# Performance work log

Measured on AMD Instinct MI355X. Metric: run time of the kernel, lower is better.

Reference implementation:

```python
import jax, jax.numpy as jnp
import numpy as np

B, N, M = 2, 256, 256  # batch items, bboxes per item, feature dim (output_channel)
BLOCKS = 2             # graph_conv_block_num


def _conv2d(x, w, b):
    # x: [C,H,W], w: [O,I,kh,kw] -> [O,H,W], SAME padding, stride 1
    y = jax.lax.conv_general_dilated(x[None], w, (1, 1), 'SAME',
                                     dimension_numbers=('NCHW', 'OIHW', 'NCHW'))
    return y[0] + b[:, None, None]


def setup_inputs() -> dict:
    key = jax.random.key(0)
    ks = jax.random.split(key, 8)
    s = 0.02  # small init to keep activations tame through conv stack
    return {
        'edge_feats': jax.random.normal(ks[0], (B, N, N, 7), jnp.float32),
        'node_feats': jax.random.normal(ks[1], (B, N, M), jnp.float32),
        'adapter_w': jax.random.normal(ks[2], (M, 7, 1, 1), jnp.float32) * s,
        'adapter_b': jnp.zeros((M,), jnp.float32),
        'conv0_w': jax.random.normal(ks[3], (M, 3 * M, 3, 3), jnp.float32) * s,
        'conv0_b': jnp.zeros((M,), jnp.float32),
        'conv1_w': jax.random.normal(ks[4], (M, M, 3, 3), jnp.float32) * s,
        'conv1_b': jnp.zeros((M,), jnp.float32),
        'last_w': jax.random.normal(ks[5], (M, M, 3, 3), jnp.float32) * s,
        'last_b': jnp.zeros((M,), jnp.float32),
        'att_w': jax.random.normal(ks[6], (1, M, 1, 1), jnp.float32) * s,
        'att_b': jnp.zeros((1,), jnp.float32),
    }


def reference(edge_feats, node_feats, adapter_w, adapter_b, conv0_w, conv0_b,
              conv1_w, conv1_b, last_w, last_b, att_w, att_b):
    def one(e, n):
        # e: [N,N,7], n: [N,M]
        edge = _conv2d(jnp.transpose(e, (2, 0, 1)), adapter_w, adapter_b)  # [M,N,N]
        node = n
        for _ in range(BLOCKS):  # conv weights shared across blocks, as in torch
            nT = node.T  # [M,N]
            # channel layout at (i,j): [node_i | edge_ij | node_j]
            feat = jnp.concatenate([
                jnp.broadcast_to(nT[:, :, None], (M, N, N)),
                edge,
                jnp.broadcast_to(nT[:, None, :], (M, N, N)),
            ], axis=0)  # [3M,N,N]
            feat = jax.nn.relu(_conv2d(feat, conv0_w, conv0_b))
            feat = jax.nn.relu(_conv2d(feat, conv1_w, conv1_b))
            # edge attention: 1x1 conv -> leaky_relu -> softmax over j -> weighted sum
            att = jax.nn.leaky_relu(_conv2d(feat, att_w, att_b))   # [1,N,N]
            coeff = jax.nn.softmax(att, axis=-1)                   # softmax over last dim
            node = jnp.sum(coeff * feat, axis=-1).T                # [N,M]
            edge = jax.nn.relu(_conv2d(feat, last_w, last_b))      # [M,N,N]
        return node, jnp.transpose(edge, (1, 2, 0))  # [N,M], [N,N,M]
    return jax.vmap(one)(edge_feats, node_feats)
```

## Files before the change

kernel.cpp:

```cpp
#include <hip/hip_runtime.h>
#include <hip/hip_bf16.h>

typedef __hip_bfloat16 bf16;
typedef __attribute__((ext_vector_type(8))) short s16x8;
typedef __attribute__((ext_vector_type(4))) float f32x4;

__device__ __forceinline__ float b2f(bf16 x) { return __bfloat162float(x); }
__device__ __forceinline__ bf16 f2b(float x) { return __float2bfloat16(x); }

#define BARRIER() do { asm volatile("" ::: "memory"); \
                       __builtin_amdgcn_s_barrier();  \
                       asm volatile("" ::: "memory"); } while (0)

__global__ __launch_bounds__(256) void fill_sentinel(float* out, int n) {
  int idx = blockIdx.x * 256 + threadIdx.x;
  if (idx < n) out[idx] = 100.0f;
}

__global__ __launch_bounds__(256) void zero_fill(bf16* z) {
  z[blockIdx.x * 256 + threadIdx.x] = f2b(0.f);
}

__global__ __launch_bounds__(256) void pack_w(const float* __restrict__ c0w,
                                              const float* __restrict__ c1w,
                                              const float* __restrict__ lw,
                                              bf16* wp0, bf16* wp1, bf16* wp2, bf16* wnp) {
  const int SEG = 9 * 256 * 256;
  int idx = blockIdx.x * 256 + threadIdx.x;
  if (idx < 3 * SEG) {
    int which = idx / SEG, r = idx % SEG;
    int s = r >> 16, o = (r >> 8) & 255, c = r & 255;
    int ky = s / 3, kx = s - 3 * ky;
    if (which == 0)      wp0[r] = f2b(c0w[(((size_t)o * 768 + 256 + c) * 3 + ky) * 3 + kx]);
    else if (which == 1) wp1[r] = f2b(c1w[(((size_t)o * 256 + c) * 3 + ky) * 3 + kx]);
    else                 wp2[r] = f2b(lw [(((size_t)o * 256 + c) * 3 + ky) * 3 + kx]);
  } else {
    int r = idx - 3 * SEG;
    int m = r & 255, c = (r >> 8) & 255, tt = r >> 16;
    int ot = tt % 3, t2 = (tt / 3) % 3, p = tt / 9;
    int ky, kx, cin;
    if (p == 0) { kx = t2; ky = ot; cin = c; }
    else        { ky = t2; kx = ot; cin = 512 + c; }
    wnp[r] = f2b(c0w[(((size_t)m * 768 + cin) * 3 + ky) * 3 + kx]);
  }
}

__global__ __launch_bounds__(256) void adapter_k(const float* __restrict__ e,
                                                 const float* __restrict__ aw,
                                                 const float* __restrict__ ab,
                                                 bf16* __restrict__ E) {
  int i = blockIdx.x;
  int m = threadIdx.x;
  __shared__ float se[256 * 7];
  const size_t rb = (size_t)i * (256 * 7);
  for (int idx = m; idx < 256 * 7; idx += 256) se[idx] = e[rb + idx];
  __syncthreads();
  float w[7];
#pragma unroll
  for (int c = 0; c < 7; ++c) w[c] = aw[m * 7 + c];
  float bias = ab[m];
  bf16* ob = E + (size_t)i * 65536 + m;
  for (int j = 0; j < 256; ++j) {
    const float* ej = se + j * 7;
    float a = bias;
#pragma unroll
    for (int c = 0; c < 7; ++c) a += w[c] * ej[c];
    ob[(size_t)j * 256] = f2b(a);
  }
}

template <typename T>
__global__ __launch_bounds__(256) void node_terms(const T* __restrict__ nd,
                                                  const bf16* __restrict__ wnp,
                                                  float* __restrict__ TT) {
  int bid = blockIdx.x;
  int chunk = bid & 63;
  int t = (bid >> 6) % 3;
  int p = bid / 192;
  int tid = threadIdx.x;
  __shared__ float snd[6][256];
  int pos0 = chunk * 4;
  for (int idx = tid; idx < 6 * 256; idx += 256) {
    int r = idx >> 8, c = idx & 255;
    int gp = pos0 - 1 + r;
    snd[r][c] = (gp >= 0 && gp < 256) ? (float)nd[(size_t)gp * 256 + c] : 0.f;
  }
  __syncthreads();
  float acc[4] = {0.f, 0.f, 0.f, 0.f};
  const bf16* wb = wnp + (size_t)((p * 3 + t) * 3) * 65536 + tid;
  for (int c = 0; c < 256; ++c) {
    float w0 = b2f(wb[(size_t)c * 256]);
    float w1 = b2f(wb[(size_t)(65536 + c * 256)]);
    float w2 = b2f(wb[(size_t)(2 * 65536 + c * 256)]);
#pragma unroll
    for (int ii = 0; ii < 4; ++ii)
      acc[ii] += w0 * snd[ii][c] + w1 * snd[ii + 1][c] + w2 * snd[ii + 2][c];
  }
  float* o = TT + (((size_t)(p * 3 + t) * 256 + pos0) * 256) + tid;
#pragma unroll
  for (int ii = 0; ii < 4; ++ii) o[(size_t)ii * 256] = acc[ii];
}

template <int EPI, int F32OUT>
__global__ __launch_bounds__(512, 1)
void conv3x3_k(const bf16* __restrict__ inb, const bf16* __restrict__ wpack,
               const float* __restrict__ bias, void* __restrict__ outv,
               const float* __restrict__ TT, const bf16* __restrict__ zrow) {
  __shared__ __align__(16) char lds[131072];
  const int bid = blockIdx.x;
  const int i = ((bid & 7) << 5) + (bid >> 3);
  const int tid = threadIdx.x;
  const int lane = tid & 63, wid = tid >> 6;
  const int wr = wid >> 2, wc = wid & 3;
  const int lo = lane & 15, hi = lane >> 4;
  const int xlane = tid >> 3;
  const int sw = ((tid & 7) ^ (xlane & 7)) << 3;
  const int g16 = (tid & 7) << 4;

  const int gxk0 = (hi ^ (lo & 7)) << 4;
  const int gxk1 = ((4 + hi) ^ (lo & 7)) << 4;
  const int aJ0 = (wr * 64 + lo) * 128 + gxk0;
  const int aJ1 = (wr * 64 + lo) * 128 + gxk1;
  const int bBase = ((wc & 1) * 64 + lo) * 128 + 65536 + (wc >> 1) * 16384;
  const int bJ0 = bBase + gxk0;
  const int bJ1 = bBase + gxk1;

  f32x4 acc00[4][2], acc01[4][2], acc10[4][2], acc11[4][2];
  const f32x4 z = {0.f, 0.f, 0.f, 0.f};
#pragma unroll
  for (int mf = 0; mf < 4; ++mf)
#pragma unroll
    for (int nf = 0; nf < 2; ++nf) { acc00[mf][nf] = z; acc01[mf][nf] = z;
                                     acc10[mf][nf] = z; acc11[mf][nf] = z; }
  s16x8 afA[4][2], bf0[2][2], bf1[2][2];
  s16x8 gi[4], gw[4];

  const bf16* rows0 = (i >= 1)   ? inb + (size_t)(i - 1) * 65536 : zrow;
  const bf16* rows1 = inb + (size_t)i * 65536;
  const bf16* rows2 = (i <= 254) ? inb + (size_t)(i + 1) * 65536 : zrow;

  auto ISSUE = [&](int t) {
    const int ky = (t >= 24) ? 2 : ((t >= 12) ? 1 : 0);
    const int rem = t - ky * 12;
    const int kx = rem >> 2, cc = rem & 3;
    const bf16* rowp = (ky == 0) ? rows0 : (ky == 1 ? rows1 : rows2);
    const int s = ky * 3 + kx;
#pragma unroll
    for (int r = 0; r < 4; ++r) {
      const int px = r * 64 + xlane;
      const int j = px + kx - 1;
      const bf16* src = (j >= 0 && j <= 255)
          ? rowp + ((size_t)j << 8) + cc * 64 + sw
          : zrow + sw;
      gi[r] = *(const s16x8*)src;
      gw[r] = *(const s16x8*)(wpack + ((size_t)s << 16) +
                              (((size_t)(r * 64 + xlane)) << 8) + cc * 64 + sw);
    }
  };
  auto WRITE_STAGE = [&](int par) {
#pragma unroll
    for (int r = 0; r < 4; ++r) {
      const int px = r * 64 + xlane;
      *(s16x8*)(lds + par * 32768 + px * 128 + g16) = gi[r];
      *(s16x8*)(lds + 65536 + par * 32768 + px * 128 + g16) = gw[r];
    }
  };
  auto LD_A = [&](int par, int mh) {
#pragma unroll
    for (int mf = 0; mf < 4; ++mf) {
      afA[mf][0] = *(const s16x8*)(lds + aJ0 + mf * 2048 + mh * 16384 + par * 32768);
      afA[mf][1] = *(const s16x8*)(lds + aJ1 + mf * 2048 + mh * 16384 + par * 32768);
    }
  };
  auto LD_B = [&](int par, int nh, s16x8 (&dst)[2][2]) {
#pragma unroll
    for (int nf = 0; nf < 2; ++nf) {
      dst[nf][0] = *(const s16x8*)(lds + bJ0 + nh * 4096 + nf * 2048 + par * 32768);
      dst[nf][1] = *(const s16x8*)(lds + bJ1 + nh * 4096 + nf * 2048 + par * 32768);
    }
  };

#define MMA_Q(ACC, BFR)                                                       \
  __builtin_amdgcn_s_setprio(1);                                              \
  _Pragma("unroll") for (int kk = 0; kk < 2; ++kk)                            \
  _Pragma("unroll") for (int mf = 0; mf < 4; ++mf)                            \
  _Pragma("unroll") for (int nf = 0; nf < 2; ++nf)                            \
    ACC[mf][nf] = __builtin_amdgcn_mfma_f32_16x16x32_bf16(                    \
        afA[mf][kk], BFR[nf][kk], ACC[mf][nf], 0, 0, 0);                      \
  __builtin_amdgcn_s_setprio(0);

  ISSUE(0);
  asm volatile("s_waitcnt vmcnt(0)" ::: "memory");
  WRITE_STAGE(0);
  asm volatile("s_waitcnt lgkmcnt(0)" ::: "memory");
  BARRIER();

#pragma unroll 1
  for (int t = 0; t < 36; ++t) {
    const int p = t & 1;
    if (t < 35) ISSUE(t + 1);
    LD_A(p, 0); LD_B(p, 0, bf0); LD_B(p, 1, bf1);
    MMA_Q(acc00, bf0);
    MMA_Q(acc01, bf1);
    LD_A(p, 1);
    MMA_Q(acc10, bf0);
    MMA_Q(acc11, bf1);
    if (t < 35) {
      asm volatile("s_waitcnt vmcnt(0)" ::: "memory");
      WRITE_STAGE(p ^ 1);
    }
    asm volatile("s_waitcnt lgkmcnt(0)" ::: "memory");
    BARRIER();
  }
#undef MMA_Q

  bf16* orow = (bf16*)outv + (size_t)i * 65536;
  float* orowf = (float*)outv + (size_t)i * 65536;
#define EPI_Q(ACC, MH, NH)                                                    \
  _Pragma("unroll") for (int mf = 0; mf < 4; ++mf) {                          \
    _Pragma("unroll") for (int nf = 0; nf < 2; ++nf) {                        \
      const int o = wc * 64 + NH * 32 + nf * 16 + lo;                         \
      const float bs = bias[o];                                               \
      float ni0 = 0.f, ni1 = 0.f, ni2 = 0.f;                                  \
      if (EPI) { const float* TI = TT + (size_t)i * 256 + o;                  \
        ni0 = TI[0]; ni1 = TI[65536]; ni2 = TI[2 * 65536]; }                  \
      _Pragma("unroll") for (int rr = 0; rr < 4; ++rr) {                      \
        const int j = MH * 128 + wr * 64 + mf * 16 + hi * 4 + rr;             \
        float v = ACC[mf][nf][rr] + bs;                                       \
        if (EPI) {                                                            \
          v += ni1 + (j > 0 ? ni0 : 0.f) + (j < 255 ? ni2 : 0.f);             \
          const float* TJ = TT + (size_t)3 * 65536 + (size_t)j * 256 + o;     \
          float nj0 = TJ[0], nj1 = TJ[65536], nj2 = TJ[2 * 65536];            \
          v += nj1 + (i > 0 ? nj0 : 0.f) + (i < 255 ? nj2 : 0.f); }           \
        v = fmaxf(v, 0.f);                                                    \
        if (F32OUT) orowf[(size_t)j * 256 + o] = v;                           \
        else        orow[(size_t)j * 256 + o] = f2b(v);                       \
      } } }
  EPI_Q(acc00, 0, 0); EPI_Q(acc01, 0, 1); EPI_Q(acc10, 1, 0); EPI_Q(acc11, 1, 1);
#undef EPI_Q
}

template <int F32OUT>
__global__ __launch_bounds__(256) void att_wsum(const bf16* __restrict__ feat,
                                                const float* __restrict__ aw,
                                                const float* __restrict__ ab,
                                                bf16* __restrict__ ndb,
                                                float* __restrict__ ndf) {
  int i = blockIdx.x;
  int tid = threadIdx.x, lane = tid & 63, w = tid >> 6;
  __shared__ float s_aw[256];
  __shared__ float s_att[256];
  __shared__ float s_red[8];
  s_aw[tid] = aw[tid];
  __syncthreads();
  float a0 = s_aw[lane * 4], a1 = s_aw[lane * 4 + 1];
  float a2 = s_aw[lane * 4 + 2], a3 = s_aw[lane * 4 + 3];
  const bf16* fb = feat + (size_t)i * 65536;
  float abv = ab[0];
  for (int jj = 0; jj < 64; ++jj) {
    int j = w * 64 + jj;
    const bf16* f = fb + (size_t)j * 256 + lane * 4;
    float v = a0 * b2f(f[0]) + a1 * b2f(f[1]) + a2 * b2f(f[2]) + a3 * b2f(f[3]);
#pragma unroll
    for (int mk = 32; mk; mk >>= 1) v += __shfl_xor(v, mk);
    if (lane == 0) { float a = v + abv; s_att[j] = a > 0.f ? a : 0.01f * a; }
  }
  __syncthreads();
  float x = s_att[tid];
  float mx = x;
#pragma unroll
  for (int mk = 32; mk; mk >>= 1) mx = fmaxf(mx, __shfl_xor(mx, mk));
  if (lane == 0) s_red[w] = mx;
  __syncthreads();
  mx = fmaxf(fmaxf(s_red[0], s_red[1]), fmaxf(s_red[2], s_red[3]));
  float e = expf(x - mx);
  float sm = e;
#pragma unroll
  for (int mk = 32; mk; mk >>= 1) sm += __shfl_xor(sm, mk);
  if (lane == 0) s_red[4 + w] = sm;
  __syncthreads();
  sm = s_red[4] + s_red[5] + s_red[6] + s_red[7];
  __syncthreads();
  s_att[tid] = e / sm;
  __syncthreads();
  float acc = 0.f;
  for (int j = 0; j < 256; ++j) acc += s_att[j] * b2f(fb[(size_t)j * 256 + tid]);
  if (F32OUT) ndf[(size_t)i * 256 + tid] = acc;
  else        ndb[(size_t)i * 256 + tid] = f2b(acc);
}

extern "C" void kernel_launch(void* const* d_in, const int* in_sizes, int n_in,
                              void* d_out, int out_size, void* d_ws, size_t ws_size,
                              hipStream_t stream) {
  const float* edge_feats = (const float*)d_in[0];
  const float* node_feats = (const float*)d_in[1];
  const float* adapter_w  = (const float*)d_in[2];
  const float* adapter_b  = (const float*)d_in[3];
  const float* conv0_w    = (const float*)d_in[4];
  const float* conv0_b    = (const float*)d_in[5];
  const float* conv1_w    = (const float*)d_in[6];
  const float* conv1_b    = (const float*)d_in[7];
  const float* last_w     = (const float*)d_in[8];
  const float* last_b     = (const float*)d_in[9];
  const float* att_w      = (const float*)d_in[10];
  const float* att_b      = (const float*)d_in[11];
  float* out = (float*)d_out;

  char* ws = (char*)d_ws;
  size_t off = 0;
  bf16* Q    = (bf16*)(ws + off); off += (size_t)256 * 256 * 256 * 2;
  bf16* WP0  = (bf16*)(ws + off); off += (size_t)9 * 65536 * 2;
  bf16* WP1  = (bf16*)(ws + off); off += (size_t)9 * 65536 * 2;
  bf16* WP2  = (bf16*)(ws + off); off += (size_t)9 * 65536 * 2;
  bf16* WNP  = (bf16*)(ws + off); off += (size_t)18 * 65536 * 2;
  float* TT  = (float*)(ws + off); off += (size_t)2 * 3 * 65536 * 4;
  bf16* ND   = (bf16*)(ws + off); off += (size_t)65536 * 2;
  bf16* ZROW = (bf16*)(ws + off); off += (size_t)65536 * 2;
  if (ws_size < off) {
    fill_sentinel<<<(out_size + 255) / 256, 256, 0, stream>>>(out, out_size);
    return;
  }

  zero_fill<<<256, 256, 0, stream>>>(ZROW);
  pack_w<<<11520, 256, 0, stream>>>(conv0_w, conv1_w, last_w, WP0, WP1, WP2, WNP);

  for (int b = 0; b < 2; ++b) {
    bf16* P = (bf16*)(out + 131072 + (size_t)b * 16777216);
    float* edge_out = out + 131072 + (size_t)b * 16777216;
    float* node_out = out + (size_t)b * 65536;
    const float* eb = edge_feats + (size_t)b * 458752;
    const float* nb = node_feats + (size_t)b * 65536;

    adapter_k<<<256, 256, 0, stream>>>(eb, adapter_w, adapter_b, P);
    node_terms<float><<<384, 256, 0, stream>>>(nb, WNP, TT);
    conv3x3_k<1, 0><<<256, 512, 0, stream>>>(P, WP0, conv0_b, Q, TT, ZROW);
    conv3x3_k<0, 0><<<256, 512, 0, stream>>>(Q, WP1, conv1_b, P, nullptr, ZROW);
    att_wsum<0><<<256, 256, 0, stream>>>(P, att_w, att_b, ND, nullptr);
    conv3x3_k<0, 0><<<256, 512, 0, stream>>>(P, WP2, last_b, Q, nullptr, ZROW);
    node_terms<bf16><<<384, 256, 0, stream>>>(ND, WNP, TT);
    conv3x3_k<1, 0><<<256, 512, 0, stream>>>(Q, WP0, conv0_b, P, TT, ZROW);
    conv3x3_k<0, 0><<<256, 512, 0, stream>>>(P, WP1, conv1_b, Q, nullptr, ZROW);
    att_wsum<1><<<256, 256, 0, stream>>>(Q, att_w, att_b, nullptr, node_out);
    conv3x3_k<0, 1><<<256, 512, 0, stream>>>(Q, WP2, last_b, edge_out, nullptr, ZROW);
  }
}
```

Measured before the change: 1.253 ms.

## Split conv3x3 across output-channel halves with 256-thread blocks and direct-to-LDS weight loads

```diff
diff --git a/kernel.cpp b/kernel.cpp
--- a/kernel.cpp
+++ b/kernel.cpp
@@ -7,6 +7,12 @@
 
 __device__ __forceinline__ float b2f(bf16 x) { return __bfloat162float(x); }
 __device__ __forceinline__ bf16 f2b(float x) { return __float2bfloat16(x); }
+
+__device__ __forceinline__ void gld16(const void* g, void* l) {
+  __builtin_amdgcn_global_load_lds((const __attribute__((address_space(1))) unsigned int*)g,
+                                   (__attribute__((address_space(3))) unsigned int*)l,
+                                   16, 0, 0);
+}
 
 #define BARRIER() do { asm volatile("" ::: "memory"); \
                        __builtin_amdgcn_s_barrier();  \
@@ -102,16 +108,18 @@
 }
 
 template <int EPI, int F32OUT>
-__global__ __launch_bounds__(512, 1)
+__global__ __launch_bounds__(256, 2)
 void conv3x3_k(const bf16* __restrict__ inb, const bf16* __restrict__ wpack,
                const float* __restrict__ bias, void* __restrict__ outv,
                const float* __restrict__ TT, const bf16* __restrict__ zrow) {
-  __shared__ __align__(16) char lds[131072];
+  __shared__ __align__(16) char lds[65536];
   const int bid = blockIdx.x;
-  const int i = ((bid & 7) << 5) + (bid >> 3);
+  const int rest = bid >> 3;
+  const int i = ((bid & 7) << 5) + (rest >> 1);
+  const int oh = rest & 1;
   const int tid = threadIdx.x;
   const int lane = tid & 63, wid = tid >> 6;
-  const int wr = wid >> 2, wc = wid & 3;
+  const int wr = wid >> 1, wc = wid & 1;
   const int lo = lane & 15, hi = lane >> 4;
   const int xlane = tid >> 3;
   const int sw = ((tid & 7) ^ (xlane & 7)) << 3;
@@ -119,11 +127,10 @@
 
   const int gxk0 = (hi ^ (lo & 7)) << 4;
   const int gxk1 = ((4 + hi) ^ (lo & 7)) << 4;
-  const int aJ0 = (wr * 64 + lo) * 128 + gxk0;
-  const int aJ1 = (wr * 64 + lo) * 128 + gxk1;
-  const int bBase = ((wc & 1) * 64 + lo) * 128 + 65536 + (wc >> 1) * 16384;
-  const int bJ0 = bBase + gxk0;
-  const int bJ1 = bBase + gxk1;
+  const int aJ0 = (wr * 128 + lo) * 128 + gxk0;
+  const int aJ1 = (wr * 128 + lo) * 128 + gxk1;
+  const int bJ0 = 32768 + (wc * 64 + lo) * 128 + gxk0;
+  const int bJ1 = 32768 + (wc * 64 + lo) * 128 + gxk1;
 
   f32x4 acc00[4][2], acc01[4][2], acc10[4][2], acc11[4][2];
   const f32x4 z = {0.f, 0.f, 0.f, 0.f};
@@ -133,50 +140,58 @@
     for (int nf = 0; nf < 2; ++nf) { acc00[mf][nf] = z; acc01[mf][nf] = z;
                                      acc10[mf][nf] = z; acc11[mf][nf] = z; }
   s16x8 afA[4][2], bf0[2][2], bf1[2][2];
-  s16x8 gi[4], gw[4];
+  s16x8 gi[8];
 
   const bf16* rows0 = (i >= 1)   ? inb + (size_t)(i - 1) * 65536 : zrow;
   const bf16* rows1 = inb + (size_t)i * 65536;
   const bf16* rows2 = (i <= 254) ? inb + (size_t)(i + 1) * 65536 : zrow;
 
-  auto ISSUE = [&](int t) {
+  auto ISSUE_IN = [&](int t) {
     const int ky = (t >= 24) ? 2 : ((t >= 12) ? 1 : 0);
     const int rem = t - ky * 12;
     const int kx = rem >> 2, cc = rem & 3;
     const bf16* rowp = (ky == 0) ? rows0 : (ky == 1 ? rows1 : rows2);
-    const int s = ky * 3 + kx;
-#pragma unroll
-    for (int r = 0; r < 4; ++r) {
-      const int px = r * 64 + xlane;
+#pragma unroll
+    for (int r = 0; r < 8; ++r) {
+      const int px = r * 32 + xlane;
       const int j = px + kx - 1;
       const bf16* src = (j >= 0 && j <= 255)
           ? rowp + ((size_t)j << 8) + cc * 64 + sw
           : zrow + sw;
       gi[r] = *(const s16x8*)src;
-      gw[r] = *(const s16x8*)(wpack + ((size_t)s << 16) +
-                              (((size_t)(r * 64 + xlane)) << 8) + cc * 64 + sw);
-    }
-  };
-  auto WRITE_STAGE = [&](int par) {
+    }
+  };
+  auto GLD_W = [&](int t, int par) {
+    const int ky = (t >= 24) ? 2 : ((t >= 12) ? 1 : 0);
+    const int rem = t - ky * 12;
+    const int kx = rem >> 2, cc = rem & 3;
+    const int s = ky * 3 + kx;
 #pragma unroll
     for (int r = 0; r < 4; ++r) {
-      const int px = r * 64 + xlane;
-      *(s16x8*)(lds + par * 32768 + px * 128 + g16) = gi[r];
-      *(s16x8*)(lds + 65536 + par * 32768 + px * 128 + g16) = gw[r];
-    }
-  };
-  auto LD_A = [&](int par, int mh) {
+      const int oc = r * 32 + xlane;
+      gld16(wpack + ((size_t)s << 16) + (((size_t)(oh * 128 + oc)) << 8) + cc * 64 + sw,
+            lds + 32768 + par * 16384 + ((r * 32 + wid * 8) << 7));
+    }
+  };
+  auto WRITE_IN = [&]() {
+#pragma unroll
+    for (int r = 0; r < 8; ++r) {
+      const int px = r * 32 + xlane;
+      *(s16x8*)(lds + px * 128 + g16) = gi[r];
+    }
+  };
+  auto LD_A = [&](int mh) {
 #pragma unroll
     for (int mf = 0; mf < 4; ++mf) {
-      afA[mf][0] = *(const s16x8*)(lds + aJ0 + mf * 2048 + mh * 16384 + par * 32768);
-      afA[mf][1] = *(const s16x8*)(lds + aJ1 + mf * 2048 + mh * 16384 + par * 32768);
+      afA[mf][0] = *(const s16x8*)(lds + aJ0 + mf * 2048 + mh * 8192);
+      afA[mf][1] = *(const s16x8*)(lds + aJ1 + mf * 2048 + mh * 8192);
     }
   };
   auto LD_B = [&](int par, int nh, s16x8 (&dst)[2][2]) {
 #pragma unroll
     for (int nf = 0; nf < 2; ++nf) {
-      dst[nf][0] = *(const s16x8*)(lds + bJ0 + nh * 4096 + nf * 2048 + par * 32768);
-      dst[nf][1] = *(const s16x8*)(lds + bJ1 + nh * 4096 + nf * 2048 + par * 32768);
+      dst[nf][0] = *(const s16x8*)(lds + bJ0 + par * 16384 + nh * 4096 + nf * 2048);
+      dst[nf][1] = *(const s16x8*)(lds + bJ1 + par * 16384 + nh * 4096 + nf * 2048);
     }
   };
 
@@ -189,25 +204,27 @@
         afA[mf][kk], BFR[nf][kk], ACC[mf][nf], 0, 0, 0);                      \
   __builtin_amdgcn_s_setprio(0);
 
-  ISSUE(0);
+  GLD_W(0, 0);
+  ISSUE_IN(0);
   asm volatile("s_waitcnt vmcnt(0)" ::: "memory");
-  WRITE_STAGE(0);
+  WRITE_IN();
   asm volatile("s_waitcnt lgkmcnt(0)" ::: "memory");
   BARRIER();
 
 #pragma unroll 1
   for (int t = 0; t < 36; ++t) {
     const int p = t & 1;
-    if (t < 35) ISSUE(t + 1);
-    LD_A(p, 0); LD_B(p, 0, bf0); LD_B(p, 1, bf1);
+    if (t < 35) { GLD_W(t + 1, p ^ 1); ISSUE_IN(t + 1); }
+    LD_A(0); LD_B(p, 0, bf0); LD_B(p, 1, bf1);
     MMA_Q(acc00, bf0);
     MMA_Q(acc01, bf1);
-    LD_A(p, 1);
+    LD_A(1);
     MMA_Q(acc10, bf0);
     MMA_Q(acc11, bf1);
+    BARRIER();
     if (t < 35) {
       asm volatile("s_waitcnt vmcnt(0)" ::: "memory");
-      WRITE_STAGE(p ^ 1);
+      WRITE_IN();
     }
     asm volatile("s_waitcnt lgkmcnt(0)" ::: "memory");
     BARRIER();
@@ -219,13 +236,13 @@
 #define EPI_Q(ACC, MH, NH)                                                    \
   _Pragma("unroll") for (int mf = 0; mf < 4; ++mf) {                          \
     _Pragma("unroll") for (int nf = 0; nf < 2; ++nf) {                        \
-      const int o = wc * 64 + NH * 32 + nf * 16 + lo;                         \
+      const int o = oh * 128 + wc * 64 + NH * 32 + nf * 16 + lo;              \
       const float bs = bias[o];                                               \
       float ni0 = 0.f, ni1 = 0.f, ni2 = 0.f;                                  \
       if (EPI) { const float* TI = TT + (size_t)i * 256 + o;                  \
         ni0 = TI[0]; ni1 = TI[65536]; ni2 = TI[2 * 65536]; }                  \
       _Pragma("unroll") for (int rr = 0; rr < 4; ++rr) {                      \
-        const int j = MH * 128 + wr * 64 + mf * 16 + hi * 4 + rr;             \
+        const int j = wr * 128 + MH * 64 + mf * 16 + hi * 4 + rr;             \
         float v = ACC[mf][nf][rr] + bs;                                       \
         if (EPI) {                                                            \
           v += ni1 + (j > 0 ? ni0 : 0.f) + (j < 255 ? ni2 : 0.f);             \
@@ -333,14 +350,14 @@
 
     adapter_k<<<256, 256, 0, stream>>>(eb, adapter_w, adapter_b, P);
     node_terms<float><<<384, 256, 0, stream>>>(nb, WNP, TT);
-    conv3x3_k<1, 0><<<256, 512, 0, stream>>>(P, WP0, conv0_b, Q, TT, ZROW);
-    conv3x3_k<0, 0><<<256, 512, 0, stream>>>(Q, WP1, conv1_b, P, nullptr, ZROW);
+    conv3x3_k<1, 0><<<512, 256, 0, stream>>>(P, WP0, conv0_b, Q, TT, ZROW);
+    conv3x3_k<0, 0><<<512, 256, 0, stream>>>(Q, WP1, conv1_b, P, nullptr, ZROW);
     att_wsum<0><<<256, 256, 0, stream>>>(P, att_w, att_b, ND, nullptr);
-    conv3x3_k<0, 0><<<256, 512, 0, stream>>>(P, WP2, last_b, Q, nullptr, ZROW);
+    conv3x3_k<0, 0><<<512, 256, 0, stream>>>(P, WP2, last_b, Q, nullptr, ZROW);
     node_terms<bf16><<<384, 256, 0, stream>>>(ND, WNP, TT);
-    conv3x3_k<1, 0><<<256, 512, 0, stream>>>(Q, WP0, conv0_b, P, TT, ZROW);
-    conv3x3_k<0, 0><<<256, 512, 0, stream>>>(P, WP1, conv1_b, Q, nullptr, ZROW);
+    conv3x3_k<1, 0><<<512, 256, 0, stream>>>(Q, WP0, conv0_b, P, TT, ZROW);
+    conv3x3_k<0, 0><<<512, 256, 0, stream>>>(P, WP1, conv1_b, Q, nullptr, ZROW);
     att_wsum<1><<<256, 256, 0, stream>>>(Q, att_w, att_b, nullptr, node_out);
-    conv3x3_k<0, 1><<<256, 512, 0, stream>>>(Q, WP2, last_b, edge_out, nullptr, ZROW);
-  }
-}
+    conv3x3_k<0, 1><<<512, 256, 0, stream>>>(Q, WP2, last_b, edge_out, nullptr, ZROW);
+  }
+}
```

Result: slower. 1.300 ms (+3.8%).
